# Kernel optimization log

Measured on AMD Instinct MI355X. Metric: run time of the kernel, lower is better.

## Reference

```python
import jax, jax.numpy as jnp
import numpy as np

B, S, DIM = 2, 2048, 2048
NH, NKV = 16, 4
HD = DIM // NH
BASE, FACTOR = 10000.0, 1.0
WINDOW, STRIDE = 256, 64


def setup_inputs() -> dict:
    key = jax.random.key(0)
    ks = jax.random.split(key, 5)
    x = jax.random.normal(ks[0], (B, S, DIM), jnp.float32)
    Wq = jax.random.normal(ks[1], (DIM, DIM), jnp.float32) * 0.02
    Wkv = jax.random.normal(ks[2], (2 * NKV * HD, DIM), jnp.float32) * 0.02
    Wo = jax.random.normal(ks[3], (DIM, DIM), jnp.float32) * 0.02
    Wr = jax.random.normal(ks[4], (NH, DIM), jnp.float32) * 0.02
    br = jnp.zeros((NH,), jnp.float32)
    return {"x": x, "Wq": Wq, "Wkv": Wkv, "Wo": Wo, "Wr": Wr, "br": br}


def _rope_cos_sin(seqlen, start_pos):
    half = HD // 2
    inv_freq = 1.0 / (BASE ** (jnp.arange(0, half, dtype=jnp.float32) * 2.0 / HD))
    inv_freq = inv_freq / FACTOR  # YaRN position interpolation; FACTOR=1 -> vanilla RoPE
    mscale = float(0.1 * np.log(FACTOR) + 1.0) if FACTOR > 1.0 else 1.0
    t = jnp.arange(start_pos, start_pos + seqlen, dtype=jnp.float32)
    freqs = t[:, None] * inv_freq[None, :]  # [S, HD/2]
    return jnp.cos(freqs) * mscale, jnp.sin(freqs) * mscale


def _apply_rope(x, cos, sin):
    # x: [B, H, S, HD]; rotate-half convention
    x1, x2 = jnp.split(x, 2, axis=-1)
    return jnp.concatenate([x1 * cos - x2 * sin, x2 * cos + x1 * sin], axis=-1)


def reference(x, Wq, Wkv, Wo, Wr, br):
    scale = 1.0 / np.sqrt(HD)
    # projections
    q = (x @ Wq.T).reshape(B, S, NH, HD).transpose(0, 2, 1, 3)        # [B,NH,S,HD]
    kv = (x @ Wkv.T).reshape(B, S, 2, NKV, HD)
    k = kv[:, :, 0].transpose(0, 2, 1, 3)                              # [B,NKV,S,HD]
    v = kv[:, :, 1].transpose(0, 2, 1, 3)
    # RoPE (start_pos = 0)
    cos, sin = _rope_cos_sin(S, 0)
    cos, sin = cos[None, None], sin[None, None]
    q = _apply_rope(q, cos, sin)
    k = _apply_rope(k, cos, sin)
    # GQA expansion (repeat_interleave over head axis)
    rep = NH // NKV
    k = jnp.repeat(k, rep, axis=1)                                     # [B,NH,S,HD]
    v = jnp.repeat(v, rep, axis=1)
    # per-head sigmoid routing gate on q
    head_w = jax.nn.sigmoid(x @ Wr.T + br)                             # [B,S,NH]
    q = q * head_w.transpose(0, 2, 1)[..., None]
    # local windowed causal attention
    qi = jnp.arange(S)[:, None]
    ki = jnp.arange(S)[None, :]
    mask = (ki <= qi) & (ki >= qi - WINDOW)                            # [S,S]
    scores = jnp.einsum('bhqd,bhkd->bhqk', q, k) * scale
    scores = jnp.where(mask, scores, -1e30)
    attn_local = jnp.einsum('bhqk,bhkd->bhqd', jax.nn.softmax(scores, axis=-1), v)
    # strided global attention (non-causal over subsampled keys)
    g_idx = jnp.arange(0, S, STRIDE)
    kg, vg = k[:, :, g_idx], v[:, :, g_idx]                            # [B,NH,S/STRIDE,HD]
    gscores = jnp.einsum('bhqd,bhkd->bhqk', q, kg) * scale
    attn_global = jnp.einsum('bhqk,bhkd->bhqd', jax.nn.softmax(gscores, axis=-1), vg)
    out = 0.7 * attn_local + 0.3 * attn_global
    out = out.transpose(0, 2, 1, 3).reshape(B, S, DIM)
    return out @ Wo.T
```

## Files before the change

### kernel.cpp

```cpp
#include <hip/hip_runtime.h>
#include <stdint.h>

typedef unsigned short u16;
typedef uint32_t u32;
typedef __bf16 bf16x8 __attribute__((ext_vector_type(8)));
typedef u16    u16x8  __attribute__((ext_vector_type(8)));
typedef float  f32x4  __attribute__((ext_vector_type(4)));
typedef u32    u32x4v __attribute__((ext_vector_type(4)));

constexpr int Bc = 2, Sc = 2048, DIMc = 2048, NHc = 16, NKVc = 4, HDc = 128;
constexpr int Mc  = Bc * Sc;
constexpr int QKVN = 3072;
constexpr float SCALE = 0.08838834764831845f;

__device__ __forceinline__ u16 f2bf(float f) {
    uint32_t u = __builtin_bit_cast(uint32_t, f);
    u += 0x7FFFu + ((u >> 16) & 1u);
    return (u16)(u >> 16);
}
__device__ __forceinline__ u32 pk2bf(float a, float b) {
    return (u32)f2bf(a) | ((u32)f2bf(b) << 16);
}

__device__ __forceinline__ void async_cp16(const u16* gsrc, u16* ldst) {
    __builtin_amdgcn_global_load_lds(
        (__attribute__((address_space(1))) void*)(gsrc),
        (__attribute__((address_space(3))) void*)(ldst), 16, 0, 0);
}

constexpr int HWB = Mc;
constexpr int CQ1 = DIMc * DIMc / 4;
constexpr int CQ2 = 1024 * DIMc / 4;
constexpr int CQ3 = DIMc * DIMc / 4;
constexpr int NWQ = (CQ1 + CQ2 + CQ3) / 256;
constexpr int NTB = Sc * 64 / 256;
__global__ __launch_bounds__(256) void cvt_hw(const float* __restrict__ x,
                                              const float* __restrict__ Wq,
                                              const float* __restrict__ Wkv,
                                              const float* __restrict__ Wo,
                                              const float* __restrict__ Wr,
                                              const float* __restrict__ br,
                                              u16* __restrict__ xb,
                                              u16* __restrict__ Wqkvb,
                                              u16* __restrict__ Wob,
                                              float* __restrict__ hw,
                                              float2* __restrict__ csT) {
    __shared__ float xs[2048];
    int bid = blockIdx.x;
    if (bid < HWB) {
        const int m = bid;
        for (int i = threadIdx.x; i < 2048; i += 256) xs[i] = x[(size_t)m * 2048 + i];
        __syncthreads();
        {
            ushort4* dst = (ushort4*)(xb + (size_t)m * 2048);
            for (int i = threadIdx.x; i < 512; i += 256) {
                float4 v = ((const float4*)xs)[i];
                ushort4 o;
                o.x = f2bf(v.x); o.y = f2bf(v.y); o.z = f2bf(v.z); o.w = f2bf(v.w);
                dst[i] = o;
            }
        }
        const int wid = threadIdx.x >> 6, lane = threadIdx.x & 63;
        for (int h = wid; h < NHc; h += 4) {
            float s = 0.f;
            for (int j = lane; j < 2048; j += 64) s += xs[j] * Wr[(size_t)h * 2048 + j];
#pragma unroll
            for (int off = 32; off; off >>= 1) s += __shfl_xor(s, off, 64);
            if (lane == 0) hw[m * NHc + h] = 1.f / (1.f + __expf(-(s + br[h])));
        }
        return;
    }
    bid -= HWB;
    if (bid < NWQ) {
        int q = bid * 256 + threadIdx.x;
        const float* src; u16* dst; int qi;
        if (q < CQ1)                 { src = Wq;  dst = Wqkvb; qi = q; }
        else if ((q -= CQ1) < CQ2)   { src = Wkv; dst = Wqkvb + (size_t)DIMc * DIMc; qi = q; }
        else                         { q -= CQ2;  src = Wo;  dst = Wob; qi = q; }
        float4 v = ((const float4*)src)[qi];
        ushort4 o;
        o.x = f2bf(v.x); o.y = f2bf(v.y); o.z = f2bf(v.z); o.w = f2bf(v.w);
        ((ushort4*)dst)[qi] = o;
        return;
    }
    bid -= NWQ;
    int idx = bid * 256 + threadIdx.x;
    int s = idx >> 6, d = idx & 63;
    float invf = powf(10000.0f, -(float)d * (1.0f / 64.0f));
    float ang = (float)s * invf;
    float2 cs;
    cs.x = cosf(ang);
    cs.y = sinf(ang);
    csT[idx] = cs;
}

__global__ __launch_bounds__(512, 2) void gemm_qkv(const u16* __restrict__ A,
                                                   const u16* __restrict__ Bw,
                                                   const float* __restrict__ hw,
                                                   const float2* __restrict__ csT,
                                                   u16* __restrict__ Qr,
                                                   u16* __restrict__ Kb,
                                                   u16* __restrict__ Vt,
                                                   u16* __restrict__ Vg) {
    __shared__ __align__(16) u16 SM[4][2][128 * 64];
    float* EpS = (float*)SM;
    const int Kd = DIMc;
    constexpr int NT = 32;
    const int tid  = threadIdx.x;
    const int lane = tid & 63;
    const int wid  = tid >> 6;
    const int m0 = blockIdx.y * 256;
    const int n0 = blockIdx.x * 256;
    const int wr = wid >> 2;
    const int wc = wid & 3;
    const int fr = lane & 15;
    const int fq = lane >> 4;
    const int f7 = fr & 7;

    const int s0 = tid, s1 = tid + 512;
    const int r0 = s0 >> 3, r1 = s1 >> 3;
    const int j0 = (s0 & 7) ^ (r0 & 7), j1 = (s1 & 7) ^ (r1 & 7);
    const u16* gA0 = A  + (size_t)(m0 + r0) * Kd + j0 * 8;
    const u16* gA1 = A  + (size_t)(m0 + r1) * Kd + j1 * 8;
    const u16* gB0 = Bw + (size_t)(n0 + r0) * Kd + j0 * 8;
    const u16* gB1 = Bw + (size_t)(n0 + r1) * Kd + j1 * 8;
    const size_t hK = (size_t)128 * Kd;

    auto stA = [&](int buf, int h, int t) {
        async_cp16(gA0 + h * hK + t * 64, &SM[buf][h][s0 * 8]);
        async_cp16(gA1 + h * hK + t * 64, &SM[buf][h][s1 * 8]);
    };
    auto stB = [&](int buf, int h, int t) {
        async_cp16(gB0 + h * hK + t * 64, &SM[2 + buf][h][s0 * 8]);
        async_cp16(gB1 + h * hK + t * 64, &SM[2 + buf][h][s1 * 8]);
    };

    f32x4 acc[8][4];
#pragma unroll
    for (int i = 0; i < 8; i++)
#pragma unroll
        for (int j = 0; j < 4; j++) {
            f32x4 z = {0.f, 0.f, 0.f, 0.f};
            acc[i][j] = z;
        }

    const int c0 = ((fq) ^ f7) * 8;
    const int c1 = ((4 + fq) ^ f7) * 8;
    bf16x8 afl[4][2], afh[4][2], bfl[2][2], bfh[2][2];

    auto rdA = [&](bf16x8 (&af)[4][2], int tb, int mh) {
        const u16* Ab = SM[tb][wr];
#pragma unroll
        for (int m2 = 0; m2 < 4; m2++) {
            int row = (mh * 4 + m2) * 16 + fr;
            af[m2][0] = __builtin_bit_cast(bf16x8, *(const u16x8*)(Ab + row * 64 + c0));
            af[m2][1] = __builtin_bit_cast(bf16x8, *(const u16x8*)(Ab + row * 64 + c1));
        }
    };
    auto rdB = [&](bf16x8 (&bf)[2][2], int tb, int nh) {
        const u16* Bb = SM[2 + tb][wc >> 1];
#pragma unroll
        for (int n2 = 0; n2 < 2; n2++) {
            int row = (wc & 1) * 64 + (nh * 2 + n2) * 16 + fr;
            bf[n2][0] = __builtin_bit_cast(bf16x8, *(const u16x8*)(Bb + row * 64 + c0));
            bf[n2][1] = __builtin_bit_cast(bf16x8, *(const u16x8*)(Bb + row * 64 + c1));
        }
    };
    auto mma = [&](bf16x8 (&af)[4][2], bf16x8 (&bf)[2][2], int mh, int nh) {
        __builtin_amdgcn_s_setprio(1);
#pragma unroll
        for (int m2 = 0; m2 < 4; m2++)
#pragma unroll
            for (int n2 = 0; n2 < 2; n2++) {
                acc[mh * 4 + m2][nh * 2 + n2] =
                    __builtin_amdgcn_mfma_f32_16x16x32_bf16(af[m2][0], bf[n2][0],
                                                            acc[mh * 4 + m2][nh * 2 + n2], 0, 0, 0);
                acc[mh * 4 + m2][nh * 2 + n2] =
                    __builtin_amdgcn_mfma_f32_16x16x32_bf16(af[m2][1], bf[n2][1],
                                                            acc[mh * 4 + m2][nh * 2 + n2], 0, 0, 0);
            }
        __builtin_amdgcn_s_setprio(0);
    };

#define LGK0 do { asm volatile("s_waitcnt lgkmcnt(0)" ::: "memory"); \
                  __builtin_amdgcn_sched_barrier(0); } while (0)
#define BAR  __builtin_amdgcn_s_barrier()

    stA(0, 0, 0); stA(0, 1, 0); stB(0, 0, 0); stB(0, 1, 0);
    stB(1, 0, 1); stB(1, 1, 1);
    asm volatile("s_waitcnt vmcnt(4)" ::: "memory");
    BAR;

#pragma unroll 1
    for (int i = 0; i < NT / 2; i++) {
        const int t0 = 2 * i, t1 = 2 * i + 1;
        rdA(afl, 0, 0); rdB(bfl, 0, 0);
        stA(1, 0, t1);
        BAR; LGK0; mma(afl, bfl, 0, 0); BAR;
        rdB(bfh, 0, 1);
        stA(1, 1, t1);
        BAR; LGK0; mma(afl, bfh, 0, 1); BAR;
        rdA(afh, 0, 1);
        if (t0 + 2 < NT) stB(0, 0, t0 + 2);
        BAR; LGK0; mma(afh, bfl, 1, 0); BAR;
        if (t0 + 2 < NT) {
            stB(0, 1, t0 + 2);
            asm volatile("s_waitcnt vmcnt(4)" ::: "memory");
        } else {
            asm volatile("s_waitcnt vmcnt(0)" ::: "memory");
        }
        BAR; __builtin_amdgcn_sched_barrier(0); mma(afh, bfh, 1, 1); BAR;
        rdA(afl, 1, 0); rdB(bfl, 1, 0);
        if (t0 + 2 < NT) stA(0, 0, t0 + 2);
        BAR; LGK0; mma(afl, bfl, 0, 0); BAR;
        rdB(bfh, 1, 1);
        if (t0 + 2 < NT) stA(0, 1, t0 + 2);
        BAR; LGK0; mma(afl, bfh, 0, 1); BAR;
        rdA(afh, 1, 1);
        if (t1 + 2 < NT) stB(1, 0, t1 + 2);
        BAR; LGK0; mma(afh, bfl, 1, 0); BAR;
        if (t1 + 2 < NT) {
            stB(1, 1, t1 + 2);
            asm volatile("s_waitcnt vmcnt(4)" ::: "memory");
        } else {
            asm volatile("s_waitcnt vmcnt(0)" ::: "memory");
        }
        BAR; __builtin_amdgcn_sched_barrier(0); mma(afh, bfh, 1, 1); BAR;
    }
#undef LGK0
#undef BAR

    const int tL = n0 >> 7;
    const int bb = m0 >> 11;
    const int sb_t = m0 & 2047;
#pragma unroll
    for (int p = 0; p < 4; p++) {
        __syncthreads();
        if (wr == (p >> 1)) {
#pragma unroll
            for (int m2 = 0; m2 < 4; m2++) {
#pragma unroll
                for (int nj = 0; nj < 4; nj++) {
                    int lr = m2 * 16 + fq * 4;
                    int col = wc * 64 + nj * 16 + fr;
#pragma unroll
                    for (int r = 0; r < 4; r++)
                        EpS[(lr + r) * 261 + col] = acc[(p & 1) * 4 + m2][nj][r];
                }
            }
        }
        __syncthreads();
        const int sbase = sb_t + p * 64;
        if (tL < 20) {
            const int d = tid & 63, rg = tid >> 6;
#pragma unroll 1
            for (int ch = 0; ch < 2; ch++) {
                const int t = tL + ch;
#pragma unroll
                for (int tt = 0; tt < 8; tt++) {
                    int lr = rg + 8 * tt;
                    int s = sbase + lr;
                    float v1 = EpS[lr * 261 + ch * 128 + d];
                    float v2 = EpS[lr * 261 + ch * 128 + 64 + d];
                    float2 cs = csT[(s << 6) + d];
                    float o1 = v1 * cs.x - v2 * cs.y;
                    float o2 = v2 * cs.x + v1 * cs.y;
                    if (t < 16) {
                        float w = hw[(size_t)((bb << 11) + s) * NHc + t] * SCALE;
                        size_t g = ((size_t)(bb * NHc + t) << 11) + s;
                        Qr[g * HDc + d]      = f2bf(o1 * w);
                        Qr[g * HDc + 64 + d] = f2bf(o2 * w);
                    } else {
                        size_t g = ((size_t)(bb * NKVc + (t - 16)) << 11) + s;
                        Kb[g * HDc + d]      = f2bf(o1);
                        Kb[g * HDc + 64 + d] = f2bf(o2);
                    }
                }
            }
        } else {
            const int sl = tid & 63, dg = tid >> 6;
            const int sg = sbase + sl;
#pragma unroll 1
            for (int ch = 0; ch < 2; ch++) {
                const int bhv = bb * NKVc + (tL + ch - 20);
                u16* Vbase = Vt + (size_t)bhv * HDc * Sc;
#pragma unroll
                for (int tt = 0; tt < 16; tt++) {
                    int d = dg + 8 * tt;
                    u16 bv = f2bf(EpS[sl * 261 + ch * 128 + d]);
                    Vbase[(size_t)d * Sc + sg] = bv;
                    if ((sg & 63) == 0)
                        Vg[(size_t)bhv * 4096 + d * 32 + (sg >> 6)] = bv;
                }
            }
        }
    }
}

__global__ __launch_bounds__(512, 2) void gemm_bt3(const u16* __restrict__ A,
                                                   const u16* __restrict__ Bw,
                                                   float* __restrict__ C,
                                                   int Mdim, int Ndim, int Kdim) {
    __shared__ __align__(16) u16 As[2][256 * 64];
    __shared__ __align__(16) u16 Bs[2][128 * 64];
    const int tid  = threadIdx.x;
    const int lane = tid & 63;
    const int wid  = tid >> 6;
    const int m0 = blockIdx.y * 256;
    const int n0 = blockIdx.x * 128;
    const int wm = (wid >> 1) * 64;
    const int wn = (wid & 1) * 64;
    const int fr = lane & 15;
    const int fq = lane >> 4;
    const int f7 = fr & 7;

    const u16* gA[4]; const u16* gB[2];
    int sOffA[4], sOffB[2];
#pragma unroll
    for (int q = 0; q < 4; q++) {
        int s = tid + q * 512;
        int row = s >> 3;
        int j = (s & 7) ^ (row & 7);
        gA[q] = A + (size_t)(m0 + row) * Kdim + j * 8;
        sOffA[q] = s * 8;
    }
#pragma unroll
    for (int q = 0; q < 2; q++) {
        int s = tid + q * 512;
        int row = s >> 3;
        int j = (s & 7) ^ (row & 7);
        gB[q] = Bw + (size_t)(n0 + row) * Kdim + j * 8;
        sOffB[q] = s * 8;
    }

    f32x4 acc[4][4];
#pragma unroll
    for (int i = 0; i < 4; i++)
#pragma unroll
        for (int j = 0; j < 4; j++) {
            f32x4 z = {0.f, 0.f, 0.f, 0.f};
            acc[i][j] = z;
        }

    const int NT = Kdim >> 6;
    const int c0 = ((fq) ^ f7) * 8;
    const int c1 = ((4 + fq) ^ f7) * 8;

#pragma unroll
    for (int q = 0; q < 4; q++) async_cp16(gA[q], &As[0][sOffA[q]]);
#pragma unroll
    for (int q = 0; q < 2; q++) async_cp16(gB[q], &Bs[0][sOffB[q]]);
#pragma unroll
    for (int q = 0; q < 4; q++) async_cp16(gA[q] + 64, &As[1][sOffA[q]]);
#pragma unroll
    for (int q = 0; q < 2; q++) async_cp16(gB[q] + 64, &Bs[1][sOffB[q]]);

    for (int t = 0; t < NT; t++) {
        const u16* At = As[t & 1];
        const u16* Bt = Bs[t & 1];

        if (t + 1 < NT) {
            asm volatile("s_waitcnt vmcnt(6)" ::: "memory");
        } else {
            asm volatile("s_waitcnt vmcnt(0)" ::: "memory");
        }
        __builtin_amdgcn_s_barrier();

        bf16x8 af0[4], bf0[4];
#pragma unroll
        for (int i = 0; i < 4; i++)
            af0[i] = __builtin_bit_cast(bf16x8, *(const u16x8*)(At + (wm + i * 16 + fr) * 64 + c0));
#pragma unroll
        for (int j = 0; j < 4; j++)
            bf0[j] = __builtin_bit_cast(bf16x8, *(const u16x8*)(Bt + (wn + j * 16 + fr) * 64 + c0));
        asm volatile("s_waitcnt lgkmcnt(0)" ::: "memory");
        __builtin_amdgcn_sched_barrier(0);
        __builtin_amdgcn_s_setprio(1);
#pragma unroll
        for (int i = 0; i < 2; i++)
#pragma unroll
            for (int j = 0; j < 4; j++)
                acc[i][j] = __builtin_amdgcn_mfma_f32_16x16x32_bf16(af0[i], bf0[j], acc[i][j], 0, 0, 0);
        __builtin_amdgcn_s_setprio(0);

        bf16x8 af1[4], bf1[4];
#pragma unroll
        for (int i = 0; i < 4; i++)
            af1[i] = __builtin_bit_cast(bf16x8, *(const u16x8*)(At + (wm + i * 16 + fr) * 64 + c1));
#pragma unroll
        for (int j = 0; j < 4; j++)
            bf1[j] = __builtin_bit_cast(bf16x8, *(const u16x8*)(Bt + (wn + j * 16 + fr) * 64 + c1));
        __builtin_amdgcn_s_setprio(1);
#pragma unroll
        for (int i = 2; i < 4; i++)
#pragma unroll
            for (int j = 0; j < 4; j++)
                acc[i][j] = __builtin_amdgcn_mfma_f32_16x16x32_bf16(af0[i], bf0[j], acc[i][j], 0, 0, 0);
        __builtin_amdgcn_s_setprio(0);
        asm volatile("s_waitcnt lgkmcnt(0)" ::: "memory");
        __builtin_amdgcn_sched_barrier(0);
        __builtin_amdgcn_s_barrier();

        if (t + 2 < NT) {
#pragma unroll
            for (int q = 0; q < 4; q++)
                async_cp16(gA[q] + (size_t)(t + 2) * 64, &As[t & 1][sOffA[q]]);
        }
        __builtin_amdgcn_s_setprio(1);
#pragma unroll
        for (int i = 0; i < 2; i++)
#pragma unroll
            for (int j = 0; j < 4; j++)
                acc[i][j] = __builtin_amdgcn_mfma_f32_16x16x32_bf16(af1[i], bf1[j], acc[i][j], 0, 0, 0);
        __builtin_amdgcn_s_setprio(0);

        if (t + 2 < NT) {
#pragma unroll
            for (int q = 0; q < 2; q++)
                async_cp16(gB[q] + (size_t)(t + 2) * 64, &Bs[t & 1][sOffB[q]]);
        }
        __builtin_amdgcn_s_setprio(1);
#pragma unroll
        for (int i = 2; i < 4; i++)
#pragma unroll
            for (int j = 0; j < 4; j++)
                acc[i][j] = __builtin_amdgcn_mfma_f32_16x16x32_bf16(af1[i], bf1[j], acc[i][j], 0, 0, 0);
        __builtin_amdgcn_s_setprio(0);
    }

#pragma unroll
    for (int i = 0; i < 4; i++)
#pragma unroll
        for (int j = 0; j < 4; j++) {
            int row = m0 + wm + i * 16 + fq * 4;
            int col = n0 + wn + j * 16 + fr;
#pragma unroll
            for (int r = 0; r < 4; r++)
                C[(size_t)(row + r) * Ndim + col] = acc[i][j][r];
        }
}

__device__ __forceinline__ float colreduce_max(f32x4 a, f32x4 b) {
    float m = fmaxf(fmaxf(fmaxf(a[0], a[1]), fmaxf(a[2], a[3])),
                    fmaxf(fmaxf(b[0], b[1]), fmaxf(b[2], b[3])));
    m = fmaxf(m, __shfl_xor(m, 16, 64));
    m = fmaxf(m, __shfl_xor(m, 32, 64));
    return m;
}

__device__ __forceinline__ bf16x8 build_pfrag(u32 pk0, u32 pk1, u32 pk2, u32 pk3, int lane) {
    const int c = lane & 15, Q = lane >> 4;
    const int sl0 = ((Q & 1) * 2) * 16 + c;
    const int sl1 = sl0 + 16;
    u32 a0 = (u32)__shfl((int)pk0, sl0, 64), b0 = (u32)__shfl((int)pk2, sl0, 64);
    u32 a1 = (u32)__shfl((int)pk1, sl0, 64), b1 = (u32)__shfl((int)pk3, sl0, 64);
    u32 a2 = (u32)__shfl((int)pk0, sl1, 64), b2 = (u32)__shfl((int)pk2, sl1, 64);
    u32 a3 = (u32)__shfl((int)pk1, sl1, 64), b3 = (u32)__shfl((int)pk3, sl1, 64);
    const bool hi = Q >= 2;
    u32x4v r = { hi ? b0 : a0, hi ? b1 : a1, hi ? b2 : a2, hi ? b3 : a3 };
    return __builtin_bit_cast(bf16x8, r);
}

__global__ __launch_bounds__(256) void attn3(const u16* __restrict__ Qr,
                                             const u16* __restrict__ Kb,
                                             const u16* __restrict__ Vt,
                                             const u16* __restrict__ Vg,
                                             u16* __restrict__ attnb) {
    __shared__ __align__(16) u16 Ksh[2 * 4096];
    __shared__ __align__(16) u16 Vsh[2 * 4096];
    const int tid  = threadIdx.x;
    const int lane = tid & 63, wid = tid >> 6;
    const int bid  = blockIdx.x;
    const int q64  = (31 - (bid >> 5)) << 6;
    const int bh   = bid & 31;
    const int h    = bh & 15;
    const int b    = bh >> 4;
    const int qw   = q64 + wid * 16;
    const int c = lane & 15, Q = lane >> 4;
    const int kvh = h >> 2;

    const u16* Qp = Qr + ((size_t)((b * NHc + h) * Sc + qw)) * HDc;
    const u16* Kh = Kb + (size_t)(b * NKVc + kvh) * Sc * HDc;
    const u16* Vh = Vt + (size_t)(b * NKVc + kvh) * HDc * Sc;
    const u16* Vgh = Vg + (size_t)(b * NKVc + kvh) * HDc * 32;

    const int kp0 = (q64 >= 256) ? (q64 - 256) : 0;
    const int nstages = (q64 + 64 - kp0) >> 5;

    auto stageLoad = [&](int bufi, int kp) {
        u16* Kd = Ksh + bufi * 4096;
        u16* Vd = Vsh + bufi * 4096;
#pragma unroll
        for (int qq = 0; qq < 2; qq++) {
            int s = tid + qq * 256;
            int kr = s >> 4;
            int jk = (s & 15) ^ (kr & 15);
            async_cp16(Kh + (size_t)(kp + kr) * HDc + jk * 8, Kd + s * 8);
            int dv = s >> 2;
            int jv = (s & 3) ^ ((dv >> 2) & 3);
            async_cp16(Vh + (size_t)dv * Sc + kp + jv * 8, Vd + s * 8);
        }
    };

    bf16x8 qf[4];
#pragma unroll
    for (int ch = 0; ch < 4; ch++)
        qf[ch] = __builtin_bit_cast(bf16x8, *(const u16x8*)(Qp + c * HDc + ch * 32 + Q * 8));

    stageLoad(0, kp0);

    f32x4 sg0 = {0.f,0.f,0.f,0.f}, sg1 = {0.f,0.f,0.f,0.f};
#pragma unroll
    for (int ch = 0; ch < 4; ch++) {
        bf16x8 k0 = __builtin_bit_cast(bf16x8, *(const u16x8*)(Kh + ((size_t)c << 6) * HDc + ch * 32 + Q * 8));
        bf16x8 k1 = __builtin_bit_cast(bf16x8, *(const u16x8*)(Kh + ((size_t)(c + 16) << 6) * HDc + ch * 32 + Q * 8));
        sg0 = __builtin_amdgcn_mfma_f32_16x16x32_bf16(k0, qf[ch], sg0, 0, 0, 0);
        sg1 = __builtin_amdgcn_mfma_f32_16x16x32_bf16(k1, qf[ch], sg1, 0, 0, 0);
    }
    float mg = colreduce_max(sg0, sg1);
    f32x4 pg0, pg1;
    float gsum = 0.f;
#pragma unroll
    for (int r = 0; r < 4; r++) {
        pg0[r] = __expf(sg0[r] - mg);
        pg1[r] = __expf(sg1[r] - mg);
        gsum += pg0[r] + pg1[r];
    }
    gsum += __shfl_xor(gsum, 16, 64);
    gsum += __shfl_xor(gsum, 32, 64);
    const float lG = gsum;
    bf16x8 pgf = build_pfrag(pk2bf(pg0[0], pg0[1]), pk2bf(pg0[2], pg0[3]),
                             pk2bf(pg1[0], pg1[1]), pk2bf(pg1[2], pg1[3]), lane);
    f32x4 OG[8];
#pragma unroll
    for (int dt = 0; dt < 8; dt++) {
        bf16x8 vf = __builtin_bit_cast(bf16x8, *(const u16x8*)(Vgh + (dt * 16 + c) * 32 + Q * 8));
        f32x4 z = {0.f, 0.f, 0.f, 0.f};
        OG[dt] = __builtin_amdgcn_mfma_f32_16x16x32_bf16(vf, pgf, z, 0, 0, 0);
    }

    f32x4 OL[8];
#pragma unroll
    for (int dt = 0; dt < 8; dt++) { f32x4 z = {0.f,0.f,0.f,0.f}; OL[dt] = z; }
    float mL = -1e30f, lL = 0.f;

    for (int ip = 0; ip < nstages; ip++) {
        const int kp = kp0 + ip * 32;
        __syncthreads();
        if (ip + 1 < nstages) stageLoad((ip + 1) & 1, kp + 32);
        const u16* Kd = Ksh + (ip & 1) * 4096;
        const u16* Vd = Vsh + (ip & 1) * 4096;

        if (kp > qw + 15 || kp + 31 < qw - 256) continue;

        f32x4 s0 = {0.f,0.f,0.f,0.f}, s1 = {0.f,0.f,0.f,0.f};
#pragma unroll
        for (int ch = 0; ch < 4; ch++) {
            int jj = ch * 4 + Q;
            bf16x8 k0 = __builtin_bit_cast(bf16x8, *(const u16x8*)(Kd + (c * 16 + (jj ^ c)) * 8));
            bf16x8 k1 = __builtin_bit_cast(bf16x8, *(const u16x8*)(Kd + ((16 + c) * 16 + (jj ^ c)) * 8));
            s0 = __builtin_amdgcn_mfma_f32_16x16x32_bf16(k0, qf[ch], s0, 0, 0, 0);
            s1 = __builtin_amdgcn_mfma_f32_16x16x32_bf16(k1, qf[ch], s1, 0, 0, 0);
        }
        if ((kp + 31 > qw) || (kp < qw - 241)) {
            const int q = qw + c;
#pragma unroll
            for (int r = 0; r < 4; r++) {
                int kk0 = kp + Q * 4 + r;
                int kk1 = kk0 + 16;
                if (kk0 > q || kk0 + 256 < q) s0[r] = -1e30f;
                if (kk1 > q || kk1 + 256 < q) s1[r] = -1e30f;
            }
        }
        float mx = colreduce_max(s0, s1);
        float mnew = fmaxf(mL, mx);
        float alpha = __expf(mL - mnew);
        f32x4 p0, p1;
        float sum = 0.f;
#pragma unroll
        for (int r = 0; r < 4; r++) {
            p0[r] = __expf(s0[r] - mnew);
            p1[r] = __expf(s1[r] - mnew);
            sum += p0[r] + p1[r];
        }
        sum += __shfl_xor(sum, 16, 64);
        sum += __shfl_xor(sum, 32, 64);
        lL = lL * alpha + sum;
        mL = mnew;
        bf16x8 pf = build_pfrag(pk2bf(p0[0], p0[1]), pk2bf(p0[2], p0[3]),
                                pk2bf(p1[0], p1[1]), pk2bf(p1[2], p1[3]), lane);
#pragma unroll
        for (int dt = 0; dt < 8; dt++) {
            int d = dt * 16 + c;
            bf16x8 vf = __builtin_bit_cast(bf16x8, *(const u16x8*)(Vd + (d * 4 + (Q ^ (c >> 2))) * 8));
            OL[dt] = OL[dt] * alpha;
            OL[dt] = __builtin_amdgcn_mfma_f32_16x16x32_bf16(vf, pf, OL[dt], 0, 0, 0);
        }
    }

    const float rL = 0.7f / lL, rG = 0.3f / lG;
    u16* orow = attnb + ((size_t)(b * Sc + qw + c)) * DIMc + h * HDc;
#pragma unroll
    for (int dt = 0; dt < 8; dt++) {
        ushort4 ov;
        ov.x = f2bf(OL[dt][0] * rL + OG[dt][0] * rG);
        ov.y = f2bf(OL[dt][1] * rL + OG[dt][1] * rG);
        ov.z = f2bf(OL[dt][2] * rL + OG[dt][2] * rG);
        ov.w = f2bf(OL[dt][3] * rL + OG[dt][3] * rG);
        *(ushort4*)(orow + dt * 16 + Q * 4) = ov;
    }
}

extern "C" void kernel_launch(void* const* d_in, const int* in_sizes, int n_in,
                              void* d_out, int out_size, void* d_ws, size_t ws_size,
                              hipStream_t stream) {
    const float* x   = (const float*)d_in[0];
    const float* Wq  = (const float*)d_in[1];
    const float* Wkv = (const float*)d_in[2];
    const float* Wo  = (const float*)d_in[3];
    const float* Wr  = (const float*)d_in[4];
    const float* br  = (const float*)d_in[5];
    float* out = (float*)d_out;

    char* p = (char*)d_ws;
    u16* xb    = (u16*)p;   p += (size_t)Mc * DIMc * 2;
    u16* Wqkvb = (u16*)p;   p += (size_t)QKVN * DIMc * 2;
    u16* Wob   = (u16*)p;   p += (size_t)DIMc * DIMc * 2;
    float* hw  = (float*)p; p += (size_t)Mc * NHc * 4;
    float2* csT = (float2*)p; p += (size_t)Sc * 64 * 8;
    u16* Qrb   = (u16*)p;   p += (size_t)Mc * DIMc * 2;
    u16* Kb16  = (u16*)p;   p += (size_t)Bc * NKVc * Sc * HDc * 2;
    u16* Vt16  = (u16*)p;   p += (size_t)Bc * NKVc * HDc * Sc * 2;
    u16* Vg16  = (u16*)p;   p += (size_t)Bc * NKVc * HDc * 32 * 2;
    u16* attnb = (u16*)p;   p += (size_t)Mc * DIMc * 2;

    cvt_hw<<<HWB + NWQ + NTB, 256, 0, stream>>>(x, Wq, Wkv, Wo, Wr, br, xb, Wqkvb, Wob, hw, csT);

    dim3 gqkv(QKVN / 256, Mc / 256);
    gemm_qkv<<<gqkv, 512, 0, stream>>>(xb, Wqkvb, hw, csT, Qrb, Kb16, Vt16, Vg16);

    attn3<<<Bc * NHc * (Sc / 64), 256, 0, stream>>>(Qrb, Kb16, Vt16, Vg16, attnb);

    dim3 go(DIMc / 128, Mc / 256);
    gemm_bt3<<<go, 512, 0, stream>>>(attnb, Wob, out, Mc, DIMc, DIMc);
}
```

Before: 331.8 us.

## Restructure prep kernel and fold Wo conversion into QKV GEMM spare blocks

Splits the per-row prep into separate x-to-bf16 conversion blocks, each handling four rows with unrolled vector loads. The gate dot products now use a layout of 16 rows by 16 heads per block with one thread per row-head pair, instead of a shared-memory pass per row. The Wo fp32-to-bf16 conversion moves out of the prep kernel into 64 extra blocks appended to the QKV GEMM grid. That grid becomes 1D with 256 blocks, so the conversion runs alongside the GEMM tiles, and the GEMM's tile index is recomputed from the flat block id. The gate computation re-reads x from global memory per head-thread instead of from shared memory, which relies on cache reuse.

```diff
diff --git a/kernel.cpp b/kernel.cpp
--- a/kernel.cpp
+++ b/kernel.cpp
@@ -28,62 +28,69 @@
         (__attribute__((address_space(3))) void*)(ldst), 16, 0, 0);
 }
 
-constexpr int HWB = Mc;
+constexpr int XCB  = Mc / 4;
+constexpr int GTB  = Mc / 16;
 constexpr int CQ1 = DIMc * DIMc / 4;
 constexpr int CQ2 = 1024 * DIMc / 4;
-constexpr int CQ3 = DIMc * DIMc / 4;
-constexpr int NWQ = (CQ1 + CQ2 + CQ3) / 256;
+constexpr int NWQ2 = (CQ1 + CQ2) / 256;
 constexpr int NTB = Sc * 64 / 256;
 __global__ __launch_bounds__(256) void cvt_hw(const float* __restrict__ x,
                                               const float* __restrict__ Wq,
                                               const float* __restrict__ Wkv,
-                                              const float* __restrict__ Wo,
                                               const float* __restrict__ Wr,
                                               const float* __restrict__ br,
                                               u16* __restrict__ xb,
                                               u16* __restrict__ Wqkvb,
-                                              u16* __restrict__ Wob,
                                               float* __restrict__ hw,
                                               float2* __restrict__ csT) {
-    __shared__ float xs[2048];
     int bid = blockIdx.x;
-    if (bid < HWB) {
-        const int m = bid;
-        for (int i = threadIdx.x; i < 2048; i += 256) xs[i] = x[(size_t)m * 2048 + i];
-        __syncthreads();
-        {
-            ushort4* dst = (ushort4*)(xb + (size_t)m * 2048);
-            for (int i = threadIdx.x; i < 512; i += 256) {
-                float4 v = ((const float4*)xs)[i];
-                ushort4 o;
-                o.x = f2bf(v.x); o.y = f2bf(v.y); o.z = f2bf(v.z); o.w = f2bf(v.w);
-                dst[i] = o;
-            }
-        }
-        const int wid = threadIdx.x >> 6, lane = threadIdx.x & 63;
-        for (int h = wid; h < NHc; h += 4) {
-            float s = 0.f;
-            for (int j = lane; j < 2048; j += 64) s += xs[j] * Wr[(size_t)h * 2048 + j];
-#pragma unroll
-            for (int off = 32; off; off >>= 1) s += __shfl_xor(s, off, 64);
-            if (lane == 0) hw[m * NHc + h] = 1.f / (1.f + __expf(-(s + br[h])));
+    if (bid < XCB) {
+        const float4* src = (const float4*)x + (size_t)bid * 2048;
+        ushort4* dst = (ushort4*)xb + (size_t)bid * 2048;
+#pragma unroll
+        for (int k = 0; k < 8; k++) {
+            float4 v = src[threadIdx.x + k * 256];
+            ushort4 o;
+            o.x = f2bf(v.x); o.y = f2bf(v.y); o.z = f2bf(v.z); o.w = f2bf(v.w);
+            dst[threadIdx.x + k * 256] = o;
         }
         return;
     }
-    bid -= HWB;
-    if (bid < NWQ) {
+    bid -= XCB;
+    if (bid < GTB) {
+        const int m0g = bid * 16;
+        const int r = threadIdx.x >> 4, h = threadIdx.x & 15;
+        const float4* xr = (const float4*)(x + (size_t)(m0g + r) * 2048);
+        const float4* wr = (const float4*)(Wr + (size_t)h * 2048);
+        float s0 = 0.f, s1 = 0.f, s2 = 0.f, s3 = 0.f;
+#pragma unroll 2
+        for (int j = 0; j < 512; j += 4) {
+            float4 a0 = xr[j + 0], w0 = wr[j + 0];
+            float4 a1 = xr[j + 1], w1 = wr[j + 1];
+            float4 a2 = xr[j + 2], w2 = wr[j + 2];
+            float4 a3 = xr[j + 3], w3 = wr[j + 3];
+            s0 += a0.x * w0.x + a0.y * w0.y + a0.z * w0.z + a0.w * w0.w;
+            s1 += a1.x * w1.x + a1.y * w1.y + a1.z * w1.z + a1.w * w1.w;
+            s2 += a2.x * w2.x + a2.y * w2.y + a2.z * w2.z + a2.w * w2.w;
+            s3 += a3.x * w3.x + a3.y * w3.y + a3.z * w3.z + a3.w * w3.w;
+        }
+        float s = (s0 + s1) + (s2 + s3) + br[h];
+        hw[(size_t)(m0g + r) * NHc + h] = 1.f / (1.f + __expf(-s));
+        return;
+    }
+    bid -= GTB;
+    if (bid < NWQ2) {
         int q = bid * 256 + threadIdx.x;
         const float* src; u16* dst; int qi;
-        if (q < CQ1)                 { src = Wq;  dst = Wqkvb; qi = q; }
-        else if ((q -= CQ1) < CQ2)   { src = Wkv; dst = Wqkvb + (size_t)DIMc * DIMc; qi = q; }
-        else                         { q -= CQ2;  src = Wo;  dst = Wob; qi = q; }
+        if (q < CQ1) { src = Wq;  dst = Wqkvb; qi = q; }
+        else         { src = Wkv; dst = Wqkvb + (size_t)DIMc * DIMc; qi = q - CQ1; }
         float4 v = ((const float4*)src)[qi];
         ushort4 o;
         o.x = f2bf(v.x); o.y = f2bf(v.y); o.z = f2bf(v.z); o.w = f2bf(v.w);
         ((ushort4*)dst)[qi] = o;
         return;
     }
-    bid -= NWQ;
+    bid -= NWQ2;
     int idx = bid * 256 + threadIdx.x;
     int s = idx >> 6, d = idx & 63;
     float invf = powf(10000.0f, -(float)d * (1.0f / 64.0f));
@@ -98,10 +105,26 @@
                                                    const u16* __restrict__ Bw,
                                                    const float* __restrict__ hw,
                                                    const float2* __restrict__ csT,
+                                                   const float* __restrict__ Wo,
+                                                   u16* __restrict__ Wob,
                                                    u16* __restrict__ Qr,
                                                    u16* __restrict__ Kb,
                                                    u16* __restrict__ Vt,
                                                    u16* __restrict__ Vg) {
+    const int bidL = blockIdx.x;
+    if (bidL >= 192) {
+        const float4* src = (const float4*)Wo;
+        ushort4* dst = (ushort4*)Wob;
+        int i0 = (bidL - 192) * 16384 + threadIdx.x;
+#pragma unroll
+        for (int k = 0; k < 32; k++) {
+            float4 v = src[i0 + k * 512];
+            ushort4 o;
+            o.x = f2bf(v.x); o.y = f2bf(v.y); o.z = f2bf(v.z); o.w = f2bf(v.w);
+            dst[i0 + k * 512] = o;
+        }
+        return;
+    }
     __shared__ __align__(16) u16 SM[4][2][128 * 64];
     float* EpS = (float*)SM;
     const int Kd = DIMc;
@@ -109,8 +132,8 @@
     const int tid  = threadIdx.x;
     const int lane = tid & 63;
     const int wid  = tid >> 6;
-    const int m0 = blockIdx.y * 256;
-    const int n0 = blockIdx.x * 256;
+    const int m0 = (bidL / 12) * 256;
+    const int n0 = (bidL % 12) * 256;
     const int wr = wid >> 2;
     const int wc = wid & 3;
     const int fr = lane & 15;
@@ -634,10 +657,9 @@
     u16* Vg16  = (u16*)p;   p += (size_t)Bc * NKVc * HDc * 32 * 2;
     u16* attnb = (u16*)p;   p += (size_t)Mc * DIMc * 2;
 
-    cvt_hw<<<HWB + NWQ + NTB, 256, 0, stream>>>(x, Wq, Wkv, Wo, Wr, br, xb, Wqkvb, Wob, hw, csT);
-
-    dim3 gqkv(QKVN / 256, Mc / 256);
-    gemm_qkv<<<gqkv, 512, 0, stream>>>(xb, Wqkvb, hw, csT, Qrb, Kb16, Vt16, Vg16);
+    cvt_hw<<<XCB + GTB + NWQ2 + NTB, 256, 0, stream>>>(x, Wq, Wkv, Wr, br, xb, Wqkvb, hw, csT);
+
+    gemm_qkv<<<256, 512, 0, stream>>>(xb, Wqkvb, hw, csT, Wo, Wob, Qrb, Kb16, Vt16, Vg16);
 
     attn3<<<Bc * NHc * (Sc / 64), 256, 0, stream>>>(Qrb, Kb16, Vt16, Vg16, attnb);
 
```

Result: no change. 334.3 us (+0.8%).
